# Performance work log

Hardware: AMD Instinct MI355X
Metric: run time of the kernel (lower is better)

Reference implementation:

```python
import jax, jax.numpy as jnp
import numpy as np

B, S, D, H, FF = 4, 2048, 768, 12, 3072
DH = D // H
EPS = 1e-5
NEG = -1e18


def setup_inputs() -> dict:
    key = jax.random.key(0)
    ks = jax.random.split(key, 12)
    xavier = lambda k, fi, fo: jax.random.uniform(k, (fi, fo), jnp.float32,
                                                  -np.sqrt(6.0 / (fi + fo)), np.sqrt(6.0 / (fi + fo)))
    return {
        "x": jax.random.normal(ks[0], (B, S, D), jnp.float32),
        "mask": jax.random.bernoulli(ks[1], 0.1, (B, S, S)),  # True = masked
        "wq": xavier(ks[2], D, D),
        "wk": xavier(ks[3], D, D),
        "wv": xavier(ks[4], D, D),
        "wo": xavier(ks[5], D, D),
        "bo": jnp.zeros((D,), jnp.float32),
        "w1": xavier(ks[6], D, FF),
        "w2": xavier(ks[7], FF, D),
        "g1": jnp.ones((D,), jnp.float32),
        "b1": jnp.zeros((D,), jnp.float32),
        "g2": jnp.ones((D,), jnp.float32),
        "b2": jnp.zeros((D,), jnp.float32),
    }


def _layernorm(x, g, b):
    mu = jnp.mean(x, axis=-1, keepdims=True)
    var = jnp.mean(jnp.square(x - mu), axis=-1, keepdims=True)
    return (x - mu) * jax.lax.rsqrt(var + EPS) * g + b


def reference(x, mask, wq, wk, wv, wo, bo, w1, w2, g1, b1, g2, b2):
    # --- self-attention sublayer (pre-LN) ---
    h = _layernorm(x, g1, b1)
    split = lambda t: t.reshape(B, S, H, DH).transpose(0, 2, 1, 3)  # [B,H,S,DH]
    q = split(h @ wq) / np.sqrt(DH)
    k = split(h @ wk)
    v = split(h @ wv)
    scores = jnp.einsum('bhqd,bhkd->bhqk', q, k)
    scores = jnp.where(mask[:, None, :, :], NEG, scores)
    weights = jax.nn.softmax(scores, axis=-1)
    ctx = jnp.einsum('bhqk,bhkd->bhqd', weights, v)
    ctx = ctx.transpose(0, 2, 1, 3).reshape(B, S, D)
    x = x + (ctx @ wo + bo)
    # --- feed-forward sublayer (pre-LN) ---
    h = _layernorm(x, g2, b2)
    y = jax.nn.relu(h @ w1) @ w2
    return x + y
```

## Files before the change

### kernel.cpp

```cpp
#include <hip/hip_runtime.h>
#include <cstdint>


typedef __bf16 bf16_t;
typedef __bf16 bf16x8 __attribute__((ext_vector_type(8)));
typedef __bf16 bf16x4 __attribute__((ext_vector_type(4)));
typedef __bf16 bf16x2 __attribute__((ext_vector_type(2)));
typedef float  f32x4  __attribute__((ext_vector_type(4)));
typedef float  f32x16 __attribute__((ext_vector_type(16)));

#define NEGF (-1e30f)
#define LOG2E 1.44269504088896340736f

__device__ __forceinline__ float exp2_fast(float x) {
  float r;
  asm("v_exp_f32 %0, %1" : "=v"(r) : "v"(x));
  return r;
}

__device__ __forceinline__ f32x4 mfma16(bf16x8 a, bf16x8 b, f32x4 c) {
  return __builtin_amdgcn_mfma_f32_16x16x32_bf16(a, b, c, 0, 0, 0);
}
__device__ __forceinline__ f32x16 mfma32(bf16x8 a, bf16x8 b, f32x16 c) {
  return __builtin_amdgcn_mfma_f32_32x32x16_bf16(a, b, c, 0, 0, 0);
}

__device__ __forceinline__ void gload16(const bf16_t* gsrc, bf16_t* lds) {
  __builtin_amdgcn_global_load_lds(
      (const __attribute__((address_space(1))) unsigned int*)(uintptr_t)gsrc,
      (__attribute__((address_space(3))) unsigned int*)(uintptr_t)lds,
      16, 0, 0);
}

__device__ __forceinline__ unsigned pk2(float a, float b) {
  bf16x2 v = {(bf16_t)a, (bf16_t)b};
  return __builtin_bit_cast(unsigned, v);
}
__device__ __forceinline__ void pl32_swap(unsigned& a, unsigned& b) {
  asm("v_permlane32_swap_b32 %0, %1" : "+v"(a), "+v"(b));
}
__device__ __forceinline__ bf16x8 frag4(unsigned w0, unsigned w1,
                                        unsigned w2, unsigned w3) {
  union { unsigned u[4]; bf16x8 v; } t;
  t.u[0] = w0; t.u[1] = w1; t.u[2] = w2; t.u[3] = w3;
  return t.v;
}

__global__ __launch_bounds__(256) void transpose_conv(
    const float* __restrict__ W, bf16_t* __restrict__ Wt, int K, int N, float scale)
{
  __shared__ float tile[32][33];
  const int n0 = blockIdx.x * 32, k0 = blockIdx.y * 32;
  const int tx = threadIdx.x, ty = threadIdx.y;
#pragma unroll
  for (int i = 0; i < 32; i += 8)
    tile[ty + i][tx] = W[(size_t)(k0 + ty + i) * N + n0 + tx];
  __syncthreads();
#pragma unroll
  for (int i = 0; i < 32; i += 8)
    Wt[(size_t)(n0 + ty + i) * K + k0 + tx] = (bf16_t)(tile[tx][ty + i] * scale);
}

__global__ __launch_bounds__(256) void pack_mask(
    const int* __restrict__ mask, unsigned int* __restrict__ bits)
{
  const int gid = blockIdx.x * 256 + threadIdx.x;
  unsigned long long bal = __ballot(mask[gid] != 0);
  if ((threadIdx.x & 63) == 0) {
    const int wbase = gid >> 5;
    bits[wbase]     = (unsigned int)bal;
    bits[wbase + 1] = (unsigned int)(bal >> 32);
  }
}

__global__ __launch_bounds__(256) void ln_kernel(
    const float* __restrict__ xin, const float* __restrict__ gamma,
    const float* __restrict__ beta, bf16_t* __restrict__ outb)
{
  __shared__ float red[8];
  const int row = blockIdx.x;
  const float* xr = xin + (size_t)row * 768;
  const int t = threadIdx.x;
  float v0 = xr[t], v1 = xr[t + 256], v2 = xr[t + 512];
  float s  = v0 + v1 + v2;
  float s2 = v0 * v0 + v1 * v1 + v2 * v2;
#pragma unroll
  for (int m = 32; m >= 1; m >>= 1) {
    s  += __shfl_xor(s, m, 64);
    s2 += __shfl_xor(s2, m, 64);
  }
  if ((t & 63) == 0) { red[t >> 6] = s; red[4 + (t >> 6)] = s2; }
  __syncthreads();
  s  = red[0] + red[1] + red[2] + red[3];
  s2 = red[4] + red[5] + red[6] + red[7];
  const float mu  = s * (1.0f / 768.0f);
  const float var = s2 * (1.0f / 768.0f) - mu * mu;
  const float rs  = rsqrtf(var + 1e-5f);
  bf16_t* orow = outb + (size_t)row * 768;
  orow[t]       = (bf16_t)((v0 - mu) * rs * gamma[t]       + beta[t]);
  orow[t + 256] = (bf16_t)((v1 - mu) * rs * gamma[t + 256] + beta[t + 256]);
  orow[t + 512] = (bf16_t)((v2 - mu) * rs * gamma[t + 512] + beta[t + 512]);
}

template <bool RELU, bool OUT_F32, bool HAS_BIAS, bool HAS_RES>
__global__ __launch_bounds__(256) void gemm_kernel(
    const bf16_t* __restrict__ A, const bf16_t* __restrict__ Bt,
    void* __restrict__ Cout, const float* __restrict__ bias,
    const float* __restrict__ res, int Mdim, int Ndim, int Kdim)
{
  __shared__ __align__(16) bf16_t Smem[2][128 * 64];
  bf16_t* const As = Smem[0];
  bf16_t* const Bs = Smem[1];
  const int tid = threadIdx.x;
  const int lane = tid & 63, w = tid >> 6;
  const int l15 = lane & 15, g = lane >> 4;
  const int gx = gridDim.x;
  const int nwg = gx * gridDim.y;
  const int p = blockIdx.y * gx + blockIdx.x;
  const int wg = (p & 7) * (nwg >> 3) + (p >> 3);
  const int bm = (wg / gx) * 128, bn = (wg % gx) * 128;
  const int wr = (w >> 1) * 64, wc = (w & 1) * 64;
  const int swz = l15 & 7;

  f32x4 acc[4][4] = {};
  const int nK = Kdim >> 6;
  for (int kt = 0; kt < nK; ++kt) {
    const int k0 = kt << 6;
#pragma unroll
    for (int it = 0; it < 4; ++it) {
      const int ch = it * 256 + tid;
      const int r = ch >> 3, c = ch & 7;
      gload16(A + (size_t)(bm + r) * Kdim + k0 + ((c ^ (r & 7)) * 8), As + ch * 8);
    }
#pragma unroll
    for (int it = 0; it < 4; ++it) {
      const int ch = it * 256 + tid;
      const int r = ch >> 3, c = ch & 7;
      gload16(Bt + (size_t)(bn + r) * Kdim + k0 + ((c ^ (r & 7)) * 8), Bs + ch * 8);
    }
    __syncthreads();
#pragma unroll
    for (int kk = 0; kk < 2; ++kk) {
      bf16x8 af[4], bfr[4];
#pragma unroll
      for (int i = 0; i < 4; ++i)
        af[i] = *(const bf16x8*)(As + (wr + i * 16 + l15) * 64 +
                                 (((kk * 4 + g) ^ swz) * 8));
#pragma unroll
      for (int j = 0; j < 4; ++j)
        bfr[j] = *(const bf16x8*)(Bs + (wc + j * 16 + l15) * 64 +
                                  (((kk * 4 + g) ^ swz) * 8));
#pragma unroll
      for (int i = 0; i < 4; ++i)
#pragma unroll
        for (int j = 0; j < 4; ++j)
          acc[i][j] = mfma16(af[i], bfr[j], acc[i][j]);
    }
    __syncthreads();
  }

  if constexpr (!OUT_F32) {
    bf16_t* const wb = &Smem[0][0] + w * 4096;
#pragma unroll
    for (int i = 0; i < 4; ++i)
#pragma unroll
      for (int j = 0; j < 4; ++j)
#pragma unroll
        for (int r = 0; r < 4; ++r) {
          const int row = i * 16 + g * 4 + r, col = j * 16 + l15;
          float v = acc[i][j][r];
          if constexpr (RELU) v = fmaxf(v, 0.f);
          *(bf16_t*)((char*)wb + row * 128 + ((col * 2) ^ ((row & 7) << 4))) =
              (bf16_t)v;
        }
    __syncthreads();
    bf16_t* const crow0 = (bf16_t*)Cout + (size_t)(bm + wr) * Ndim + bn + wc;
    const int c = lane & 7;
#pragma unroll
    for (int ps = 0; ps < 8; ++ps) {
      const int row = (lane >> 3) + ps * 8;
      bf16x8 v = *(const bf16x8*)((char*)wb + row * 128 +
                                  ((c * 16) ^ ((row & 7) << 4)));
      *(bf16x8*)(crow0 + (size_t)row * Ndim + c * 8) = v;
    }
  } else {
    float* const fb = (float*)&Smem[0][0] + w * 2048;
    const int c = lane & 7;
#pragma unroll
    for (int jh = 0; jh < 2; ++jh) {
      if (jh) __syncthreads();
#pragma unroll
      for (int i = 0; i < 4; ++i)
#pragma unroll
        for (int jj = 0; jj < 2; ++jj)
#pragma unroll
          for (int r = 0; r < 4; ++r) {
            const int row = i * 16 + g * 4 + r, col = jj * 16 + l15;
            *(float*)((char*)fb + row * 128 + ((col * 4) ^ ((row & 7) << 4))) =
                acc[i][jh * 2 + jj][r];
          }
      __syncthreads();
      const int gcol = bn + wc + jh * 32 + c * 4;
      float4 bv = {0.f, 0.f, 0.f, 0.f};
      if constexpr (HAS_BIAS) bv = *(const float4*)(bias + gcol);
#pragma unroll
      for (int ps = 0; ps < 8; ++ps) {
        const int row = (lane >> 3) + ps * 8;
        float4 v = *(const float4*)((char*)fb + row * 128 +
                                    ((c * 16) ^ ((row & 7) << 4)));
        if constexpr (HAS_BIAS) { v.x += bv.x; v.y += bv.y; v.z += bv.z; v.w += bv.w; }
        if constexpr (HAS_RES) {
          const float4 rv = *(const float4*)(res + (size_t)(bm + wr + row) * Ndim + gcol);
          v.x += rv.x; v.y += rv.y; v.z += rv.z; v.w += rv.w;
        }
        *(float4*)((float*)Cout + (size_t)(bm + wr + row) * Ndim + gcol) = v;
      }
    }
  }
}

__global__ __launch_bounds__(256) void transpose_v(
    const bf16_t* __restrict__ qkv, bf16_t* __restrict__ vT)
{
  __shared__ bf16_t t[64][66];
  const int st = blockIdx.x;
  const int bh = blockIdx.y;
  const int b = bh / 12, h = bh % 12;
  const int tid = threadIdx.x;
#pragma unroll
  for (int it = 0; it < 2; ++it) {
    const int ch = it * 256 + tid;
    const int r = ch >> 3, c = ch & 7;
    bf16x8 vv = *(const bf16x8*)(qkv + (size_t)(b * 2048 + st * 64 + r) * 2304 +
                                 1536 + h * 64 + c * 8);
#pragma unroll
    for (int j = 0; j < 8; ++j) t[r][c * 8 + j] = vv[j];
  }
  __syncthreads();
#pragma unroll
  for (int it = 0; it < 2; ++it) {
    const int ch = it * 256 + tid;
    const int d = ch >> 3, c = ch & 7;
    bf16x8 o;
#pragma unroll
    for (int j = 0; j < 8; ++j) o[j] = t[c * 8 + j][d];
    *(bf16x8*)(vT + (size_t)(bh * 64 + d) * 2048 + st * 64 + c * 8) = o;
  }
}

__global__ __launch_bounds__(256, 4) void attn_kernel(
    const bf16_t* __restrict__ qkv, const bf16_t* __restrict__ vT,
    const unsigned int* __restrict__ mbits, bf16_t* __restrict__ ctx)
{
  __shared__ __align__(16) bf16_t KsBuf[2][64 * 64];
  __shared__ __align__(16) bf16_t VsBuf[2][64 * 64];
  const int tid = threadIdx.x;
  const int lane = tid & 63, w = tid >> 6;
  const int q32 = lane & 31, hi = lane >> 5;
  const int bh = blockIdx.x;
  const int qt = blockIdx.y;
  const int b = bh / 12, h = bh % 12;
  const int qrow0 = qt * 128 + w * 32;
  const int qabs = qrow0 + q32;

  bf16x8 qf[4];
#pragma unroll
  for (int c = 0; c < 4; ++c)
    qf[c] = *(const bf16x8*)(qkv + (size_t)(b * 2048 + qabs) * 2304 +
                             h * 64 + c * 16 + hi * 8);

  auto stage = [&](bf16_t* ks, bf16_t* vs, int kt) {
    const size_t kb0 = (size_t)(b * 2048 + kt * 64);
#pragma unroll
    for (int it = 0; it < 2; ++it) {
      const int ch = it * 256 + tid;
      const int r = ch >> 3, c = ch & 7;
      gload16(qkv + (kb0 + r) * 2304 + 768 + h * 64 + ((c ^ (r & 7)) * 8), ks + ch * 8);
    }
#pragma unroll
    for (int it = 0; it < 2; ++it) {
      const int ch = it * 256 + tid;
      const int r = ch >> 3, c = ch & 7;
      gload16(vT + (size_t)(bh * 64 + r) * 2048 + kt * 64 + ((c ^ (r & 7)) * 8),
              vs + ch * 8);
    }
  };

  f32x16 oacc[2] = {};
  float mrun = NEGF, lrun = 0.f;

  stage(KsBuf[0], VsBuf[0], 0);
  __syncthreads();

  for (int kt = 0; kt < 32; ++kt) {
    const bf16_t* ksc = (kt & 1) ? KsBuf[1] : KsBuf[0];
    const bf16_t* vsc = (kt & 1) ? VsBuf[1] : VsBuf[0];
    if (kt < 31)
      stage((kt & 1) ? KsBuf[0] : KsBuf[1], (kt & 1) ? VsBuf[0] : VsBuf[1], kt + 1);

    const uint2 mm = *(const uint2*)(mbits + (size_t)(b * 2048 + qabs) * 64 + kt * 2);
    const unsigned mwv[2] = {mm.x >> (hi * 4), mm.y >> (hi * 4)};

    f32x16 sacc[2] = {};
#pragma unroll
    for (int c = 0; c < 4; ++c) {
#pragma unroll
      for (int kb = 0; kb < 2; ++kb) {
        const int row = kb * 32 + q32;
        const int slot = (2 * c + hi) ^ (row & 7);
        bf16x8 kf = *(const bf16x8*)(ksc + row * 64 + slot * 8);
        sacc[kb] = mfma32(kf, qf[c], sacc[kb]);
      }
    }

    float rmax = NEGF;
#pragma unroll
    for (int kb = 0; kb < 2; ++kb)
#pragma unroll
      for (int i = 0; i < 16; ++i) rmax = fmaxf(rmax, sacc[kb][i]);
    rmax = fmaxf(rmax, __shfl_xor(rmax, 32, 64));
    if (!__all(rmax - mrun <= 8.f)) {
      const float mn = fmaxf(mrun, rmax);
      const float sc = exp2_fast(mrun - mn);
      lrun *= sc;
      oacc[0] *= sc;
      oacc[1] *= sc;
      mrun = mn;
    }
    float ps = 0.f;
#pragma unroll
    for (int kb = 0; kb < 2; ++kb) {
#pragma unroll
      for (int rq = 0; rq < 4; ++rq) {
        const unsigned sel = mwv[kb] >> (8 * rq);
#pragma unroll
        for (int i = 0; i < 4; ++i) {
          const float e = exp2_fast(sacc[kb][rq * 4 + i] - mrun);
          const float p = ((sel >> i) & 1u) ? 0.f : e;
          sacc[kb][rq * 4 + i] = p;
          ps += p;
        }
      }
    }
    ps += __shfl_xor(ps, 32, 64);
    lrun += ps;

#pragma unroll
    for (int kb = 0; kb < 2; ++kb) {
      unsigned u0 = pk2(sacc[kb][0],  sacc[kb][1]);
      unsigned u1 = pk2(sacc[kb][2],  sacc[kb][3]);
      unsigned u2 = pk2(sacc[kb][4],  sacc[kb][5]);
      unsigned u3 = pk2(sacc[kb][6],  sacc[kb][7]);
      unsigned u4 = pk2(sacc[kb][8],  sacc[kb][9]);
      unsigned u5 = pk2(sacc[kb][10], sacc[kb][11]);
      unsigned u6 = pk2(sacc[kb][12], sacc[kb][13]);
      unsigned u7 = pk2(sacc[kb][14], sacc[kb][15]);
      pl32_swap(u0, u2);  pl32_swap(u1, u3);
      pl32_swap(u4, u6);  pl32_swap(u5, u7);
      bf16x8 p0 = frag4(u0, u1, u2, u3);
      bf16x8 p1 = frag4(u4, u5, u6, u7);
#pragma unroll
      for (int ks = 0; ks < 2; ++ks) {
        const bf16x8 pf = ks ? p1 : p0;
        const int cg = kb * 4 + ks * 2 + hi;
#pragma unroll
        for (int dt = 0; dt < 2; ++dt) {
          const int row = dt * 32 + q32;
          bf16x8 vf = *(const bf16x8*)(vsc + row * 64 + ((cg ^ (row & 7)) * 8));
          oacc[dt] = mfma32(vf, pf, oacc[dt]);
        }
      }
    }
    __syncthreads();
  }

  const float inv = (lrun > 0.f) ? 1.f / lrun : 0.f;
  bf16_t* crow = ctx + (size_t)(b * 2048 + qabs) * 768 + h * 64;
#pragma unroll
  for (int dt = 0; dt < 2; ++dt)
#pragma unroll
    for (int rq = 0; rq < 4; ++rq) {
      bf16x4 ov = {(bf16_t)(oacc[dt][rq * 4 + 0] * inv),
                   (bf16_t)(oacc[dt][rq * 4 + 1] * inv),
                   (bf16_t)(oacc[dt][rq * 4 + 2] * inv),
                   (bf16_t)(oacc[dt][rq * 4 + 3] * inv)};
      *(bf16x4*)(crow + dt * 32 + rq * 8 + hi * 4) = ov;
    }
}

extern "C" void kernel_launch(void* const* d_in, const int* in_sizes, int n_in,
                              void* d_out, int out_size, void* d_ws, size_t ws_size,
                              hipStream_t stream) {
  const float* x  = (const float*)d_in[0];
  const int* mask = (const int*)d_in[1];
  const float* wq = (const float*)d_in[2];
  const float* wk = (const float*)d_in[3];
  const float* wv = (const float*)d_in[4];
  const float* wo = (const float*)d_in[5];
  const float* bo = (const float*)d_in[6];
  const float* w1 = (const float*)d_in[7];
  const float* w2 = (const float*)d_in[8];
  const float* g1 = (const float*)d_in[9];
  const float* b1 = (const float*)d_in[10];
  const float* g2 = (const float*)d_in[11];
  const float* b2 = (const float*)d_in[12];
  float* out = (float*)d_out;

  char* p = (char*)d_ws;
  bf16_t* WQKVT = (bf16_t*)p; p += (size_t)2304 * 768 * 2;
  bf16_t* WOT   = (bf16_t*)p; p += (size_t)768 * 768 * 2;
  bf16_t* W1T   = (bf16_t*)p; p += (size_t)3072 * 768 * 2;
  bf16_t* W2T   = (bf16_t*)p; p += (size_t)768 * 3072 * 2;
  unsigned int* MB = (unsigned int*)p; p += (size_t)4 * 2048 * 64 * 4;
  bf16_t* Hbuf  = (bf16_t*)p; p += (size_t)8192 * 768 * 2;
  float*  X2    = (float*)p;  p += (size_t)8192 * 768 * 4;
  bf16_t* QKV   = (bf16_t*)p; p += (size_t)8192 * 2304 * 2;
  bf16_t* CTX   = (bf16_t*)p;
  bf16_t* FFN   = QKV;
  bf16_t* VT    = Hbuf;

  const dim3 tb(32, 8);
  transpose_conv<<<dim3(24, 24), tb, 0, stream>>>(wq, WQKVT,              768, 768, 0.125f * LOG2E);
  transpose_conv<<<dim3(24, 24), tb, 0, stream>>>(wk, WQKVT + 768 * 768,  768, 768, 1.f);
  transpose_conv<<<dim3(24, 24), tb, 0, stream>>>(wv, WQKVT + 1536 * 768, 768, 768, 1.f);
  transpose_conv<<<dim3(24, 24), tb, 0, stream>>>(wo, WOT, 768, 768, 1.f);
  transpose_conv<<<dim3(96, 24), tb, 0, stream>>>(w1, W1T, 768, 3072, 1.f);
  transpose_conv<<<dim3(24, 96), tb, 0, stream>>>(w2, W2T, 3072, 768, 1.f);
  pack_mask<<<65536, 256, 0, stream>>>(mask, MB);

  ln_kernel<<<8192, 256, 0, stream>>>(x, g1, b1, Hbuf);
  gemm_kernel<false, false, false, false><<<dim3(18, 64), 256, 0, stream>>>(
      Hbuf, WQKVT, QKV, nullptr, nullptr, 8192, 2304, 768);
  transpose_v<<<dim3(32, 48), 256, 0, stream>>>(QKV, VT);
  attn_kernel<<<dim3(48, 16), 256, 0, stream>>>(QKV, VT, MB, CTX);
  gemm_kernel<false, true, true, true><<<dim3(6, 64), 256, 0, stream>>>(
      CTX, WOT, X2, bo, x, 8192, 768, 768);

  ln_kernel<<<8192, 256, 0, stream>>>(X2, g2, b2, Hbuf);
  gemm_kernel<true, false, false, false><<<dim3(24, 64), 256, 0, stream>>>(
      Hbuf, W1T, FFN, nullptr, nullptr, 8192, 3072, 768);
  gemm_kernel<false, true, false, true><<<dim3(6, 64), 256, 0, stream>>>(
      FFN, W2T, out, nullptr, X2, 8192, 768, 3072);
}
```

Before: 316.1 us.

## Fuse weight prep launches, vectorize mask/LN, write transposed V from QKV GEMM

```diff
diff --git a/kernel.cpp b/kernel.cpp
--- a/kernel.cpp
+++ b/kernel.cpp
@@ -46,67 +46,89 @@
   return t.v;
 }
 
-__global__ __launch_bounds__(256) void transpose_conv(
-    const float* __restrict__ W, bf16_t* __restrict__ Wt, int K, int N, float scale)
+__global__ __launch_bounds__(256) void prep_weights(
+    const float* __restrict__ wq, const float* __restrict__ wk,
+    const float* __restrict__ wv, const float* __restrict__ wo,
+    const float* __restrict__ w1, const float* __restrict__ w2,
+    bf16_t* __restrict__ dst)
 {
   __shared__ float tile[32][33];
-  const int n0 = blockIdx.x * 32, k0 = blockIdx.y * 32;
-  const int tx = threadIdx.x, ty = threadIdx.y;
+  const int id = blockIdx.x;
+  const float* W; size_t doff; int K, N, tx, local; float scale = 1.f;
+  if (id < 576)       { W = wq; doff = 0;       K = 768;  N = 768;  tx = 24; local = id;        scale = 0.125f * LOG2E; }
+  else if (id < 1152) { W = wk; doff = 589824;  K = 768;  N = 768;  tx = 24; local = id - 576;  }
+  else if (id < 1728) { W = wv; doff = 1179648; K = 768;  N = 768;  tx = 24; local = id - 1152; }
+  else if (id < 2304) { W = wo; doff = 1769472; K = 768;  N = 768;  tx = 24; local = id - 1728; }
+  else if (id < 4608) { W = w1; doff = 2359296; K = 768;  N = 3072; tx = 96; local = id - 2304; }
+  else                { W = w2; doff = 4718592; K = 3072; N = 768;  tx = 24; local = id - 4608; }
+  const int n0 = (local % tx) * 32, k0 = (local / tx) * 32;
+  const int tx_ = threadIdx.x, ty_ = threadIdx.y;
 #pragma unroll
   for (int i = 0; i < 32; i += 8)
-    tile[ty + i][tx] = W[(size_t)(k0 + ty + i) * N + n0 + tx];
+    tile[ty_ + i][tx_] = W[(size_t)(k0 + ty_ + i) * N + n0 + tx_];
   __syncthreads();
+  bf16_t* const Wt = dst + doff;
 #pragma unroll
   for (int i = 0; i < 32; i += 8)
-    Wt[(size_t)(n0 + ty + i) * K + k0 + tx] = (bf16_t)(tile[tx][ty + i] * scale);
+    Wt[(size_t)(n0 + ty_ + i) * K + k0 + tx_] = (bf16_t)(tile[tx_][ty_ + i] * scale);
 }
 
 __global__ __launch_bounds__(256) void pack_mask(
     const int* __restrict__ mask, unsigned int* __restrict__ bits)
 {
-  const int gid = blockIdx.x * 256 + threadIdx.x;
-  unsigned long long bal = __ballot(mask[gid] != 0);
-  if ((threadIdx.x & 63) == 0) {
-    const int wbase = gid >> 5;
-    bits[wbase]     = (unsigned int)bal;
-    bits[wbase + 1] = (unsigned int)(bal >> 32);
-  }
+  const int gid4 = blockIdx.x * 256 + threadIdx.x;
+  const int4 v = ((const int4*)mask)[gid4];
+  unsigned nib = (v.x != 0 ? 1u : 0u) | (v.y != 0 ? 2u : 0u) |
+                 (v.z != 0 ? 4u : 0u) | (v.w != 0 ? 8u : 0u);
+  nib <<= ((threadIdx.x & 7) * 4);
+  nib |= __shfl_xor((int)nib, 1, 64);
+  nib |= __shfl_xor((int)nib, 2, 64);
+  nib |= __shfl_xor((int)nib, 4, 64);
+  if ((threadIdx.x & 7) == 0) bits[gid4 >> 3] = nib;
 }
 
 __global__ __launch_bounds__(256) void ln_kernel(
     const float* __restrict__ xin, const float* __restrict__ gamma,
     const float* __restrict__ beta, bf16_t* __restrict__ outb)
 {
-  __shared__ float red[8];
-  const int row = blockIdx.x;
+  const int w = threadIdx.x >> 6, lane = threadIdx.x & 63;
+  const int row = blockIdx.x * 4 + w;
   const float* xr = xin + (size_t)row * 768;
-  const int t = threadIdx.x;
-  float v0 = xr[t], v1 = xr[t + 256], v2 = xr[t + 512];
-  float s  = v0 + v1 + v2;
-  float s2 = v0 * v0 + v1 * v1 + v2 * v2;
-#pragma unroll
-  for (int m = 32; m >= 1; m >>= 1) {
+  float4 v[3];
+  float s = 0.f, s2 = 0.f;
+#pragma unroll
+  for (int p = 0; p < 3; ++p) {
+    v[p] = *(const float4*)(xr + p * 256 + lane * 4);
+    s  += v[p].x + v[p].y + v[p].z + v[p].w;
+    s2 += v[p].x * v[p].x + v[p].y * v[p].y + v[p].z * v[p].z + v[p].w * v[p].w;
+  }
+#pragma unroll
+  for (int m = 1; m <= 32; m <<= 1) {
     s  += __shfl_xor(s, m, 64);
     s2 += __shfl_xor(s2, m, 64);
   }
-  if ((t & 63) == 0) { red[t >> 6] = s; red[4 + (t >> 6)] = s2; }
-  __syncthreads();
-  s  = red[0] + red[1] + red[2] + red[3];
-  s2 = red[4] + red[5] + red[6] + red[7];
   const float mu  = s * (1.0f / 768.0f);
   const float var = s2 * (1.0f / 768.0f) - mu * mu;
   const float rs  = rsqrtf(var + 1e-5f);
   bf16_t* orow = outb + (size_t)row * 768;
-  orow[t]       = (bf16_t)((v0 - mu) * rs * gamma[t]       + beta[t]);
-  orow[t + 256] = (bf16_t)((v1 - mu) * rs * gamma[t + 256] + beta[t + 256]);
-  orow[t + 512] = (bf16_t)((v2 - mu) * rs * gamma[t + 512] + beta[t + 512]);
-}
-
-template <bool RELU, bool OUT_F32, bool HAS_BIAS, bool HAS_RES>
+#pragma unroll
+  for (int p = 0; p < 3; ++p) {
+    const float4 g4 = *(const float4*)(gamma + p * 256 + lane * 4);
+    const float4 b4 = *(const float4*)(beta  + p * 256 + lane * 4);
+    bf16x4 o = {(bf16_t)((v[p].x - mu) * rs * g4.x + b4.x),
+                (bf16_t)((v[p].y - mu) * rs * g4.y + b4.y),
+                (bf16_t)((v[p].z - mu) * rs * g4.z + b4.z),
+                (bf16_t)((v[p].w - mu) * rs * g4.w + b4.w)};
+    *(bf16x4*)(orow + p * 256 + lane * 4) = o;
+  }
+}
+
+template <bool RELU, bool OUT_F32, bool HAS_BIAS, bool HAS_RES, bool VOUT>
 __global__ __launch_bounds__(256) void gemm_kernel(
     const bf16_t* __restrict__ A, const bf16_t* __restrict__ Bt,
     void* __restrict__ Cout, const float* __restrict__ bias,
-    const float* __restrict__ res, int Mdim, int Ndim, int Kdim)
+    const float* __restrict__ res, int Mdim, int Ndim, int Kdim,
+    bf16_t* __restrict__ vout)
 {
   __shared__ __align__(16) bf16_t Smem[2][128 * 64];
   bf16_t* const As = Smem[0];
@@ -161,27 +183,54 @@
 
   if constexpr (!OUT_F32) {
     bf16_t* const wb = &Smem[0][0] + w * 4096;
-#pragma unroll
-    for (int i = 0; i < 4; ++i)
-#pragma unroll
-      for (int j = 0; j < 4; ++j)
-#pragma unroll
-        for (int r = 0; r < 4; ++r) {
-          const int row = i * 16 + g * 4 + r, col = j * 16 + l15;
-          float v = acc[i][j][r];
-          if constexpr (RELU) v = fmaxf(v, 0.f);
-          *(bf16_t*)((char*)wb + row * 128 + ((col * 2) ^ ((row & 7) << 4))) =
-              (bf16_t)v;
-        }
-    __syncthreads();
-    bf16_t* const crow0 = (bf16_t*)Cout + (size_t)(bm + wr) * Ndim + bn + wc;
-    const int c = lane & 7;
-#pragma unroll
-    for (int ps = 0; ps < 8; ++ps) {
-      const int row = (lane >> 3) + ps * 8;
-      bf16x8 v = *(const bf16x8*)((char*)wb + row * 128 +
-                                  ((c * 16) ^ ((row & 7) << 4)));
-      *(bf16x8*)(crow0 + (size_t)row * Ndim + c * 8) = v;
+    if (VOUT && bn >= 1536) {
+#pragma unroll
+      for (int i = 0; i < 4; ++i)
+#pragma unroll
+        for (int j = 0; j < 4; ++j)
+#pragma unroll
+          for (int r = 0; r < 4; ++r) {
+            const int srow = i * 16 + g * 4 + r;
+            const int d = j * 16 + l15;
+            *(bf16_t*)((char*)wb + d * 128 + ((srow * 2) ^ ((d & 7) << 4))) =
+                (bf16_t)acc[i][j][r];
+          }
+      __syncthreads();
+      const int b = bm >> 11;
+      const int h = (bn + wc - 1536) >> 6;
+      const int s0 = (bm & 2047) + wr;
+      const int c = lane & 7;
+#pragma unroll
+      for (int ps = 0; ps < 8; ++ps) {
+        const int drow = (lane >> 3) + ps * 8;
+        bf16x8 v = *(const bf16x8*)((char*)wb + drow * 128 +
+                                    ((c * 16) ^ ((drow & 7) << 4)));
+        *(bf16x8*)(vout + ((size_t)((b * 12 + h) * 64 + drow)) * 2048 +
+                   s0 + c * 8) = v;
+      }
+    } else {
+#pragma unroll
+      for (int i = 0; i < 4; ++i)
+#pragma unroll
+        for (int j = 0; j < 4; ++j)
+#pragma unroll
+          for (int r = 0; r < 4; ++r) {
+            const int row = i * 16 + g * 4 + r, col = j * 16 + l15;
+            float v = acc[i][j][r];
+            if constexpr (RELU) v = fmaxf(v, 0.f);
+            *(bf16_t*)((char*)wb + row * 128 + ((col * 2) ^ ((row & 7) << 4))) =
+                (bf16_t)v;
+          }
+      __syncthreads();
+      bf16_t* const crow0 = (bf16_t*)Cout + (size_t)(bm + wr) * Ndim + bn + wc;
+      const int c = lane & 7;
+#pragma unroll
+      for (int ps = 0; ps < 8; ++ps) {
+        const int row = (lane >> 3) + ps * 8;
+        bf16x8 v = *(const bf16x8*)((char*)wb + row * 128 +
+                                    ((c * 16) ^ ((row & 7) << 4)));
+        *(bf16x8*)(crow0 + (size_t)row * Ndim + c * 8) = v;
+      }
     }
   } else {
     float* const fb = (float*)&Smem[0][0] + w * 2048;
@@ -216,35 +265,6 @@
         *(float4*)((float*)Cout + (size_t)(bm + wr + row) * Ndim + gcol) = v;
       }
     }
-  }
-}
-
-__global__ __launch_bounds__(256) void transpose_v(
-    const bf16_t* __restrict__ qkv, bf16_t* __restrict__ vT)
-{
-  __shared__ bf16_t t[64][66];
-  const int st = blockIdx.x;
-  const int bh = blockIdx.y;
-  const int b = bh / 12, h = bh % 12;
-  const int tid = threadIdx.x;
-#pragma unroll
-  for (int it = 0; it < 2; ++it) {
-    const int ch = it * 256 + tid;
-    const int r = ch >> 3, c = ch & 7;
-    bf16x8 vv = *(const bf16x8*)(qkv + (size_t)(b * 2048 + st * 64 + r) * 2304 +
-                                 1536 + h * 64 + c * 8);
-#pragma unroll
-    for (int j = 0; j < 8; ++j) t[r][c * 8 + j] = vv[j];
-  }
-  __syncthreads();
-#pragma unroll
-  for (int it = 0; it < 2; ++it) {
-    const int ch = it * 256 + tid;
-    const int d = ch >> 3, c = ch & 7;
-    bf16x8 o;
-#pragma unroll
-    for (int j = 0; j < 8; ++j) o[j] = t[c * 8 + j][d];
-    *(bf16x8*)(vT + (size_t)(bh * 64 + d) * 2048 + st * 64 + c * 8) = o;
   }
 }
 
@@ -260,8 +280,7 @@
   const int bh = blockIdx.x;
   const int qt = blockIdx.y;
   const int b = bh / 12, h = bh % 12;
-  const int qrow0 = qt * 128 + w * 32;
-  const int qabs = qrow0 + q32;
+  const int qabs = qt * 128 + w * 32 + q32;
 
   bf16x8 qf[4];
 #pragma unroll
@@ -417,28 +436,21 @@
   bf16_t* QKV   = (bf16_t*)p; p += (size_t)8192 * 2304 * 2;
   bf16_t* CTX   = (bf16_t*)p;
   bf16_t* FFN   = QKV;
-  bf16_t* VT    = Hbuf;
-
-  const dim3 tb(32, 8);
-  transpose_conv<<<dim3(24, 24), tb, 0, stream>>>(wq, WQKVT,              768, 768, 0.125f * LOG2E);
-  transpose_conv<<<dim3(24, 24), tb, 0, stream>>>(wk, WQKVT + 768 * 768,  768, 768, 1.f);
-  transpose_conv<<<dim3(24, 24), tb, 0, stream>>>(wv, WQKVT + 1536 * 768, 768, 768, 1.f);
-  transpose_conv<<<dim3(24, 24), tb, 0, stream>>>(wo, WOT, 768, 768, 1.f);
-  transpose_conv<<<dim3(96, 24), tb, 0, stream>>>(w1, W1T, 768, 3072, 1.f);
-  transpose_conv<<<dim3(24, 96), tb, 0, stream>>>(w2, W2T, 3072, 768, 1.f);
-  pack_mask<<<65536, 256, 0, stream>>>(mask, MB);
-
-  ln_kernel<<<8192, 256, 0, stream>>>(x, g1, b1, Hbuf);
-  gemm_kernel<false, false, false, false><<<dim3(18, 64), 256, 0, stream>>>(
-      Hbuf, WQKVT, QKV, nullptr, nullptr, 8192, 2304, 768);
-  transpose_v<<<dim3(32, 48), 256, 0, stream>>>(QKV, VT);
+  bf16_t* VT    = (bf16_t*)X2;
+
+  prep_weights<<<6912, dim3(32, 8), 0, stream>>>(wq, wk, wv, wo, w1, w2, WQKVT);
+  pack_mask<<<16384, 256, 0, stream>>>(mask, MB);
+
+  ln_kernel<<<2048, 256, 0, stream>>>(x, g1, b1, Hbuf);
+  gemm_kernel<false, false, false, false, true><<<dim3(18, 64), 256, 0, stream>>>(
+      Hbuf, WQKVT, QKV, nullptr, nullptr, 8192, 2304, 768, VT);
   attn_kernel<<<dim3(48, 16), 256, 0, stream>>>(QKV, VT, MB, CTX);
-  gemm_kernel<false, true, true, true><<<dim3(6, 64), 256, 0, stream>>>(
-      CTX, WOT, X2, bo, x, 8192, 768, 768);
-
-  ln_kernel<<<8192, 256, 0, stream>>>(X2, g2, b2, Hbuf);
-  gemm_kernel<true, false, false, false><<<dim3(24, 64), 256, 0, stream>>>(
-      Hbuf, W1T, FFN, nullptr, nullptr, 8192, 3072, 768);
-  gemm_kernel<false, true, false, true><<<dim3(6, 64), 256, 0, stream>>>(
-      FFN, W2T, out, nullptr, X2, 8192, 768, 3072);
-}
+  gemm_kernel<false, true, true, true, false><<<dim3(6, 64), 256, 0, stream>>>(
+      CTX, WOT, X2, bo, x, 8192, 768, 768, nullptr);
+
+  ln_kernel<<<2048, 256, 0, stream>>>(X2, g2, b2, Hbuf);
+  gemm_kernel<true, false, false, false, false><<<dim3(24, 64), 256, 0, stream>>>(
+      Hbuf, W1T, FFN, nullptr, nullptr, 8192, 3072, 768, nullptr);
+  gemm_kernel<false, true, false, true, false><<<dim3(6, 64), 256, 0, stream>>>(
+      FFN, W2T, out, nullptr, X2, 8192, 768, 3072, nullptr);
+}
```

After: 284.1 us. 1.11x faster.
